# Kernel optimization log

Measured on AMD Instinct MI355X. Metric: run time of the kernel, lower is better.

The kernel has to match this reference:

```python
import jax, jax.numpy as jnp
import numpy as np

B, S, D, H = 4, 2048, 1024, 16
DK = D // H


def setup_inputs() -> dict:
    key = jax.random.key(0)
    ks = jax.random.split(key, 5)
    scale = 1.0 / np.sqrt(D)
    return {
        "x": jax.random.normal(ks[0], (B, S, D), dtype=jnp.float32),
        "mask": jnp.ones((1, 1, S, S), dtype=bool),
        "Wq": jax.random.normal(ks[1], (D, D), dtype=jnp.float32) * scale,
        "Wk": jax.random.normal(ks[2], (D, D), dtype=jnp.float32) * scale,
        "Wv": jax.random.normal(ks[3], (D, D), dtype=jnp.float32) * scale,
        "Wo": jax.random.normal(ks[4], (D, D), dtype=jnp.float32) * scale,
    }


def reference(x, mask, Wq, Wk, Wv, Wo):
    # nn.Linear(d_model, d_model, bias=False): y = x @ W.T
    q = jnp.einsum('bsd,ed->bse', x, Wq).reshape(B, S, H, DK).transpose(0, 2, 1, 3)
    k = jnp.einsum('bsd,ed->bse', x, Wk).reshape(B, S, H, DK).transpose(0, 2, 1, 3)
    v = jnp.einsum('bsd,ed->bse', x, Wv).reshape(B, S, H, DK).transpose(0, 2, 1, 3)
    # scaled dot-product attention: [B,H,S,S]
    scores = jnp.einsum('bhqd,bhkd->bhqk', q, k) / jnp.sqrt(jnp.float32(DK))
    scores = jnp.where(mask, scores, jnp.float32(-1e9))
    attn = jax.nn.softmax(scores, axis=-1)
    out = jnp.einsum('bhqk,bhkd->bhqd', attn, v)  # [B,H,S,DK]
    out = out.transpose(0, 2, 1, 3).reshape(B, S, D)
    return jnp.einsum('bsd,ed->bse', out, Wo)
```

## Files before the change

### kernel.cpp

```cpp
#include <hip/hip_runtime.h>

typedef __bf16 bf16x8 __attribute__((ext_vector_type(8)));
typedef float f32x4 __attribute__((ext_vector_type(4)));
typedef float f32x16 __attribute__((ext_vector_type(16)));
typedef unsigned short u16;
typedef unsigned short u16x8 __attribute__((ext_vector_type(8)));
typedef unsigned short u16x4 __attribute__((ext_vector_type(4)));
typedef unsigned int u32;
typedef unsigned int u32x4 __attribute__((ext_vector_type(4)));

#define MFMA16(a, b, c) __builtin_amdgcn_mfma_f32_16x16x32_bf16(a, b, c, 0, 0, 0)
#define MFMA32(a, b, c) __builtin_amdgcn_mfma_f32_32x32x16_bf16(a, b, c, 0, 0, 0)

#if defined(__has_builtin)
#if __has_builtin(__builtin_amdgcn_exp2f)
#define EXP2(x) __builtin_amdgcn_exp2f(x)
#endif
#endif
#ifndef EXP2
#define EXP2(x) exp2f(x)
#endif

constexpr int NB = 4, NH = 16, SEQ = 2048, DM = 1024, DKH = 64;
constexpr int MTOT = NB * SEQ;
constexpr size_t QKV_ELEMS = (size_t)MTOT * DM;
constexpr size_t W_ELEMS = (size_t)DM * DM;
constexpr float QSCALE = 0.125f * 1.44269504088896340736f;

__device__ __forceinline__ int swz(int row, int col, int rowlen) {
  return (row * rowlen + col) ^ ((row & 7) << 3);
}

__device__ __forceinline__ void gload16(const u16* g, u16* l) {
  __builtin_amdgcn_global_load_lds(
      (const __attribute__((address_space(1))) void*)g,
      (__attribute__((address_space(3))) void*)l, 16, 0, 0);
}

__device__ __forceinline__ u32 cvtpk(float lo, float hi) {
  u32 r;
  asm("v_cvt_pk_bf16_f32 %0, %1, %2" : "=v"(r) : "v"(lo), "v"(hi));
  return r;
}
__device__ __forceinline__ void plswap(u32& a, u32& b) {
  asm volatile("v_permlane32_swap_b32 %0, %1" : "+v"(a), "+v"(b));
}

__global__ __launch_bounds__(256) void convert_bf16(
    const float* __restrict__ X, const float* __restrict__ Wq,
    const float* __restrict__ Wk, const float* __restrict__ Wv,
    const float* __restrict__ Wo, u16* __restrict__ Xb,
    u16* __restrict__ Wqb, u16* __restrict__ Wkb, u16* __restrict__ Wvb,
    u16* __restrict__ Wob) {
  const int bid = blockIdx.x;
  const float* src;
  u16* dst;
  size_t base;
  if (bid < 4096) {
    src = X; dst = Xb; base = (size_t)bid * 2048;
  } else {
    const int t = (bid - 4096) >> 9, r = (bid - 4096) & 511;
    src = (t == 0) ? Wq : (t == 1) ? Wk : (t == 2) ? Wv : Wo;
    dst = (t == 0) ? Wqb : (t == 1) ? Wkb : (t == 2) ? Wvb : Wob;
    base = (size_t)r * 2048;
  }
  const size_t e = base + (size_t)threadIdx.x * 8;
  const float4 a = *reinterpret_cast<const float4*>(src + e);
  const float4 b = *reinterpret_cast<const float4*>(src + e + 4);
  bf16x8 v;
  v[0] = (__bf16)a.x; v[1] = (__bf16)a.y; v[2] = (__bf16)a.z; v[3] = (__bf16)a.w;
  v[4] = (__bf16)b.x; v[5] = (__bf16)b.y; v[6] = (__bf16)b.z; v[7] = (__bf16)b.w;
  *reinterpret_cast<bf16x8*>(dst + e) = v;
}

__global__ __launch_bounds__(256) void gemm_qkv(
    const u16* __restrict__ A, const u16* __restrict__ Wqb,
    const u16* __restrict__ Wkb, const u16* __restrict__ Wvb,
    u16* __restrict__ Qb, u16* __restrict__ Kb, u16* __restrict__ Vtb) {
  constexpr int BM = 128, BK = 64, NT = DM / BK;
  __shared__ __align__(16) u16 As[2][BM * BK];
  __shared__ __align__(16) u16 Bs[2][BM * BK];

  const int mode = blockIdx.y >> 3;
  const u16* B = (mode == 0) ? Wqb : (mode == 1) ? Wkb : Wvb;
  u16* Yz = (mode == 0) ? Qb : (mode == 1) ? Kb : Vtb;

  const int tid = threadIdx.x;
  const int lane = tid & 63, w = tid >> 6;
  const int ln = lane & 15, lg = lane >> 4;
  const int wr = (w >> 1) * 64, wc = (w & 1) * 64;
  const int m0 = blockIdx.x * BM, n0 = (blockIdx.y & 7) * BM;

  const int srow = tid >> 3;
  const int sgg = (tid & 7) ^ (srow & 7);
  const size_t aoff = (size_t)(m0 + srow) * DM + sgg * 8;
  const size_t boff = (size_t)(n0 + srow) * DM + sgg * 8;
  const int lbase = w * 512;

  f32x4 acc[4][4];
#pragma unroll
  for (int i = 0; i < 4; ++i)
#pragma unroll
    for (int j = 0; j < 4; ++j) acc[i][j] = (f32x4){0.f, 0.f, 0.f, 0.f};

  auto stage = [&](int bsel, int k0) {
#pragma unroll
    for (int c = 0; c < 4; ++c) {
      gload16(A + aoff + (size_t)c * 32 * DM + k0, &As[bsel][c * 2048 + lbase]);
      gload16(B + boff + (size_t)c * 32 * DM + k0, &Bs[bsel][c * 2048 + lbase]);
    }
  };

  stage(0, 0);
  __syncthreads();

  int buf = 0;
  for (int t = 0; t < NT; ++t) {
    if (t + 1 < NT) stage(buf ^ 1, (t + 1) * BK);
    if (mode == 2) {
#pragma unroll
      for (int kc = 0; kc < 2; ++kc) {
        bf16x8 af[4], bfr[4];
#pragma unroll
        for (int i = 0; i < 4; ++i)
          af[i] = *reinterpret_cast<const bf16x8*>(
              &As[buf][swz(wr + i * 16 + ln, kc * 32 + lg * 8, BK)]);
#pragma unroll
        for (int j = 0; j < 4; ++j)
          bfr[j] = *reinterpret_cast<const bf16x8*>(
              &Bs[buf][swz(wc + j * 16 + ln, kc * 32 + lg * 8, BK)]);
#pragma unroll
        for (int i = 0; i < 4; ++i)
#pragma unroll
          for (int j = 0; j < 4; ++j) acc[i][j] = MFMA16(af[i], bfr[j], acc[i][j]);
      }
    } else {
#pragma unroll
      for (int kc = 0; kc < 2; ++kc) {
        bf16x8 af[4], bfr[4];
#pragma unroll
        for (int i = 0; i < 4; ++i)
          af[i] = *reinterpret_cast<const bf16x8*>(
              &As[buf][swz(wr + i * 16 + ln, kc * 32 + lg * 8, BK)]);
#pragma unroll
        for (int j = 0; j < 4; ++j)
          bfr[j] = *reinterpret_cast<const bf16x8*>(
              &Bs[buf][swz(wc + j * 16 + ln, kc * 32 + lg * 8, BK)]);
#pragma unroll
        for (int i = 0; i < 4; ++i)
#pragma unroll
          for (int j = 0; j < 4; ++j) acc[i][j] = MFMA16(bfr[j], af[i], acc[i][j]);
      }
    }
    __syncthreads();
    buf ^= 1;
  }

  if (mode == 2) {
#pragma unroll
    for (int i = 0; i < 4; ++i) {
      const int mB = m0 + wr + i * 16 + lg * 4;
      const int bb = mB >> 11, s0 = mB & (SEQ - 1);
#pragma unroll
      for (int j = 0; j < 4; ++j) {
        const int n = n0 + wc + j * 16 + ln;
        const int h = n >> 6, dk = n & 63;
        u16x4 ov;
#pragma unroll
        for (int r = 0; r < 4; ++r)
          ov[r] = __builtin_bit_cast(u16, (__bf16)acc[i][j][r]);
        *reinterpret_cast<u16x4*>(
            &Yz[(((size_t)(bb * NH + h)) * DKH + dk) * SEQ + s0]) = ov;
      }
    }
  } else {
    const float sc = (mode == 0) ? QSCALE : 1.0f;
#pragma unroll
    for (int i = 0; i < 4; ++i) {
      const int m = m0 + wr + i * 16 + ln;
      const int bb = m >> 11, s = m & (SEQ - 1);
#pragma unroll
      for (int j = 0; j < 4; ++j) {
        const int nb = n0 + wc + j * 16 + lg * 4;
        const int h = nb >> 6, dk0 = nb & 63;
        u16x4 ov;
#pragma unroll
        for (int r = 0; r < 4; ++r)
          ov[r] = __builtin_bit_cast(u16, (__bf16)(acc[i][j][r] * sc));
        *reinterpret_cast<u16x4*>(
            &Yz[(((size_t)(bb * NH + h)) * SEQ + s) * DKH + dk0]) = ov;
      }
    }
  }
}

__global__ __launch_bounds__(256) void gemm_out(
    const u16* __restrict__ A, const u16* __restrict__ B,
    float* __restrict__ Out) {
  constexpr int BM = 128, BK = 64, NT = DM / BK;
  __shared__ __align__(16) u16 As[2][BM * BK];
  __shared__ __align__(16) u16 Bs[2][BM * BK];

  const int tid = threadIdx.x;
  const int lane = tid & 63, w = tid >> 6;
  const int ln = lane & 15, lg = lane >> 4;
  const int wr = (w >> 1) * 64, wc = (w & 1) * 64;
  const int m0 = blockIdx.x * BM, n0 = blockIdx.y * BM;

  const int srow = tid >> 3;
  const int sgg = (tid & 7) ^ (srow & 7);
  const size_t aoff = (size_t)(m0 + srow) * DM + sgg * 8;
  const size_t boff = (size_t)(n0 + srow) * DM + sgg * 8;
  const int lbase = w * 512;

  f32x4 acc[4][4];
#pragma unroll
  for (int i = 0; i < 4; ++i)
#pragma unroll
    for (int j = 0; j < 4; ++j) acc[i][j] = (f32x4){0.f, 0.f, 0.f, 0.f};

  auto stage = [&](int bsel, int k0) {
#pragma unroll
    for (int c = 0; c < 4; ++c) {
      gload16(A + aoff + (size_t)c * 32 * DM + k0, &As[bsel][c * 2048 + lbase]);
      gload16(B + boff + (size_t)c * 32 * DM + k0, &Bs[bsel][c * 2048 + lbase]);
    }
  };

  stage(0, 0);
  __syncthreads();

  int buf = 0;
  for (int t = 0; t < NT; ++t) {
    if (t + 1 < NT) stage(buf ^ 1, (t + 1) * BK);
#pragma unroll
    for (int kc = 0; kc < 2; ++kc) {
      bf16x8 af[4], bfr[4];
#pragma unroll
      for (int i = 0; i < 4; ++i)
        af[i] = *reinterpret_cast<const bf16x8*>(
            &As[buf][swz(wr + i * 16 + ln, kc * 32 + lg * 8, BK)]);
#pragma unroll
      for (int j = 0; j < 4; ++j)
        bfr[j] = *reinterpret_cast<const bf16x8*>(
            &Bs[buf][swz(wc + j * 16 + ln, kc * 32 + lg * 8, BK)]);
#pragma unroll
      for (int i = 0; i < 4; ++i)
#pragma unroll
        for (int j = 0; j < 4; ++j) acc[i][j] = MFMA16(bfr[j], af[i], acc[i][j]);
    }
    __syncthreads();
    buf ^= 1;
  }

#pragma unroll
  for (int i = 0; i < 4; ++i) {
    const int m = m0 + wr + i * 16 + ln;
#pragma unroll
    for (int j = 0; j < 4; ++j) {
      const int nb = n0 + wc + j * 16 + lg * 4;
      float4 v = {acc[i][j][0], acc[i][j][1], acc[i][j][2], acc[i][j][3]};
      *reinterpret_cast<float4*>(&Out[(size_t)m * DM + nb]) = v;
    }
  }
}

__global__ __launch_bounds__(256, 4) void attn_fwd(
    const u16* __restrict__ Qg, const u16* __restrict__ Kg,
    const u16* __restrict__ Vg, u16* __restrict__ Og) {
  constexpr int KVB = 64, NT = SEQ / KVB;
  const int bid = blockIdx.x;
  const int xcd = bid & 7, grp = bid >> 3;
  const int bh = xcd * 8 + (grp >> 4), qt = grp & 15;
  const int b = bh >> 4, h = bh & 15;
  const int tid = threadIdx.x, lane = tid & 63, wv = tid >> 6;
  const int l31 = lane & 31, hi = lane >> 5;
  const size_t hoff = (size_t)bh * SEQ * DKH;
  const u16* __restrict__ Qh = Qg + hoff;
  const u16* __restrict__ Kh = Kg + hoff;
  const u16* __restrict__ Vth = Vg + hoff;

  __shared__ __align__(16) u16 Ks[2][8 * 512];
  __shared__ __align__(16) u16 Vs[2][8 * 512];

  const int qbase = qt * 128 + wv * 32;

  bf16x8 qf[4];
#pragma unroll
  for (int c = 0; c < 4; ++c)
    qf[c] = *reinterpret_cast<const bf16x8*>(
        Qh + (size_t)(qbase + l31) * DKH + c * 16 + hi * 8);

  bf16x8 ones;
#pragma unroll
  for (int e = 0; e < 8; ++e) ones[e] = (__bf16)1.0f;

  float mrow = -1e30f;
  f32x16 ot[2], lacc;
#pragma unroll
  for (int i = 0; i < 16; ++i) { ot[0][i] = 0.f; ot[1][i] = 0.f; lacc[i] = 0.f; }

  const u16* sK0 = Kh + (size_t)l31 * DKH + wv * 16 + hi * 8;
  const u16* sK1 = sK0 + 32 * DKH;
  const u16* sV0 = Vth + (size_t)l31 * SEQ + wv * 16 + hi * 8;
  const u16* sV1 = sV0 + (size_t)32 * SEQ;

  auto stage = [&](int bsel, int kv0) {
    gload16(sK0 + (size_t)kv0 * DKH, &Ks[bsel][wv * 512]);
    gload16(sK1 + (size_t)kv0 * DKH, &Ks[bsel][(wv + 4) * 512]);
    gload16(sV0 + kv0, &Vs[bsel][wv * 512]);
    gload16(sV1 + kv0, &Vs[bsel][(wv + 4) * 512]);
  };

  stage(0, 0);
  __syncthreads();

  int buf = 0;
  for (int t = 0; t < NT; ++t) {
    if (t + 1 < NT) stage(buf ^ 1, (t + 1) * KVB);
    const u16* ksb = Ks[buf];
    const u16* vsb = Vs[buf];

    f32x16 sf[2];
#pragma unroll
    for (int i = 0; i < 16; ++i) { sf[0][i] = 0.f; sf[1][i] = 0.f; }

    __builtin_amdgcn_s_setprio(1);
#pragma unroll
    for (int ks = 0; ks < 2; ++ks)
#pragma unroll
      for (int c = 0; c < 4; ++c) {
        bf16x8 ka = *reinterpret_cast<const bf16x8*>(
            &ksb[(ks * 4 + c) * 512 + lane * 8]);
        sf[ks] = MFMA32(ka, qf[c], sf[ks]);
      }
    __builtin_amdgcn_s_setprio(0);

    float t8[8];
#pragma unroll
    for (int i = 0; i < 8; ++i)
      t8[i] = fmaxf(fmaxf(sf[0][i], sf[0][i + 8]),
                    fmaxf(sf[1][i], sf[1][i + 8]));
    float ta = fmaxf(fmaxf(t8[0], t8[1]), t8[2]);
    float tb = fmaxf(fmaxf(t8[3], t8[4]), t8[5]);
    float tc = fmaxf(fmaxf(t8[6], t8[7]), ta);
    float pm = fmaxf(tb, tc);
    pm = fmaxf(pm, __shfl_xor(pm, 32));

    if (__any(pm > mrow + 8.f)) {
      const float mn = fmaxf(mrow, pm);
      const float corr = EXP2(mrow - mn);
      mrow = mn;
      lacc *= corr;
      ot[0] *= corr;
      ot[1] *= corr;
    }
    sf[0] = sf[0] - mrow;
    sf[1] = sf[1] - mrow;
#pragma unroll
    for (int ks = 0; ks < 2; ++ks)
#pragma unroll
      for (int i = 0; i < 16; ++i) sf[ks][i] = EXP2(sf[ks][i]);

#pragma unroll
    for (int ks = 0; ks < 2; ++ks) {
#pragma unroll
      for (int hk = 0; hk < 2; ++hk) {
        u32 wA0 = cvtpk(sf[ks][8 * hk + 0], sf[ks][8 * hk + 1]);
        u32 wA1 = cvtpk(sf[ks][8 * hk + 2], sf[ks][8 * hk + 3]);
        u32 wB0 = cvtpk(sf[ks][8 * hk + 4], sf[ks][8 * hk + 5]);
        u32 wB1 = cvtpk(sf[ks][8 * hk + 6], sf[ks][8 * hk + 7]);
        plswap(wA0, wB0);
        plswap(wA1, wB1);
        u32x4 pw;
        pw[0] = wA0; pw[1] = wA1; pw[2] = wB0; pw[3] = wB1;
        const bf16x8 pb = __builtin_bit_cast(bf16x8, pw);
        const int kc = ks * 2 + hk;
        __builtin_amdgcn_s_setprio(1);
        bf16x8 va0 = *reinterpret_cast<const bf16x8*>(
            &vsb[(0 * 4 + kc) * 512 + lane * 8]);
        bf16x8 va1 = *reinterpret_cast<const bf16x8*>(
            &vsb[(1 * 4 + kc) * 512 + lane * 8]);
        ot[0] = MFMA32(va0, pb, ot[0]);
        ot[1] = MFMA32(va1, pb, ot[1]);
        lacc = MFMA32(ones, pb, lacc);
        __builtin_amdgcn_s_setprio(0);
      }
    }

    __syncthreads();
    buf ^= 1;
  }

  const float inv = 1.f / lacc[0];
  const int q = qbase + l31;
#pragma unroll
  for (int ds = 0; ds < 2; ++ds)
#pragma unroll
    for (int blk = 0; blk < 4; ++blk) {
      u16x4 ov;
#pragma unroll
      for (int r = 0; r < 4; ++r)
        ov[r] = __builtin_bit_cast(u16, (__bf16)(ot[ds][blk * 4 + r] * inv));
      const int d0 = ds * 32 + blk * 8 + hi * 4;
      *reinterpret_cast<u16x4*>(
          &Og[((size_t)(b * SEQ + q)) * DM + h * DKH + d0]) = ov;
    }
}

extern "C" void kernel_launch(void* const* d_in, const int* in_sizes, int n_in,
                              void* d_out, int out_size, void* d_ws, size_t ws_size,
                              hipStream_t stream) {
  const float* x  = (const float*)d_in[0];
  const float* Wq = (const float*)d_in[2];
  const float* Wk = (const float*)d_in[3];
  const float* Wv = (const float*)d_in[4];
  const float* Wo = (const float*)d_in[5];
  float* out = (float*)d_out;

  u16* Xb  = (u16*)d_ws;
  u16* Wqb = Xb + QKV_ELEMS;
  u16* Wkb = Wqb + W_ELEMS;
  u16* Wvb = Wkb + W_ELEMS;
  u16* Wob = Wvb + W_ELEMS;
  u16* Kb  = Wob + W_ELEMS;
  u16* Vtb = Kb + QKV_ELEMS;
  u16* Qb  = (u16*)d_out;
  u16* Obuf = Xb;

  convert_bf16<<<6144, 256, 0, stream>>>(x, Wq, Wk, Wv, Wo,
                                         Xb, Wqb, Wkb, Wvb, Wob);
  gemm_qkv<<<dim3(MTOT / 128, 24), 256, 0, stream>>>(Xb, Wqb, Wkb, Wvb,
                                                     Qb, Kb, Vtb);
  attn_fwd<<<dim3(NB * NH * 16), 256, 0, stream>>>(Qb, Kb, Vtb, Obuf);
  gemm_out<<<dim3(MTOT / 128, DM / 128), 256, 0, stream>>>(Obuf, Wob, out);
}
```

Baseline: 208.8 us.

## Use 512-thread attention blocks with 4-stage KV ring and one barrier per tile

Each attention block now has 8 waves and covers 256 query rows, so K/V tiles loaded into shared memory are shared by twice as many waves, which halves the global K/V traffic per query. The double buffer becomes a 4-slot ring with three tiles in flight, using explicit vmcnt waits and a single barrier per iteration in place of two __syncthreads. The cost is larger LDS per block (64KB), fewer blocks in the grid, and correctness that depends on the hand-counted vmcnt values matching the issued loads.

```diff
diff --git a/kernel.cpp b/kernel.cpp
--- a/kernel.cpp
+++ b/kernel.cpp
@@ -265,13 +265,13 @@
   }
 }
 
-__global__ __launch_bounds__(256, 4) void attn_fwd(
+__global__ __launch_bounds__(512, 4) void attn_fwd(
     const u16* __restrict__ Qg, const u16* __restrict__ Kg,
     const u16* __restrict__ Vg, u16* __restrict__ Og) {
   constexpr int KVB = 64, NT = SEQ / KVB;
   const int bid = blockIdx.x;
   const int xcd = bid & 7, grp = bid >> 3;
-  const int bh = xcd * 8 + (grp >> 4), qt = grp & 15;
+  const int bh = xcd * 8 + (grp >> 3), qt = grp & 7;
   const int b = bh >> 4, h = bh & 15;
   const int tid = threadIdx.x, lane = tid & 63, wv = tid >> 6;
   const int l31 = lane & 31, hi = lane >> 5;
@@ -280,10 +280,10 @@
   const u16* __restrict__ Kh = Kg + hoff;
   const u16* __restrict__ Vth = Vg + hoff;
 
-  __shared__ __align__(16) u16 Ks[2][8 * 512];
-  __shared__ __align__(16) u16 Vs[2][8 * 512];
-
-  const int qbase = qt * 128 + wv * 32;
+  __shared__ __align__(16) u16 Ks[4][8 * 512];
+  __shared__ __align__(16) u16 Vs[4][8 * 512];
+
+  const int qbase = qt * 256 + wv * 32;
 
   bf16x8 qf[4];
 #pragma unroll
@@ -300,26 +300,30 @@
 #pragma unroll
   for (int i = 0; i < 16; ++i) { ot[0][i] = 0.f; ot[1][i] = 0.f; lacc[i] = 0.f; }
 
-  const u16* sK0 = Kh + (size_t)l31 * DKH + wv * 16 + hi * 8;
-  const u16* sK1 = sK0 + 32 * DKH;
-  const u16* sV0 = Vth + (size_t)l31 * SEQ + wv * 16 + hi * 8;
-  const u16* sV1 = sV0 + (size_t)32 * SEQ;
+  const u16* sK = Kh + (size_t)((wv >> 2) * 32 + l31) * DKH + (wv & 3) * 16 + hi * 8;
+  const u16* sV = Vth + (size_t)((wv >> 2) * 32 + l31) * SEQ + (wv & 3) * 16 + hi * 8;
 
   auto stage = [&](int bsel, int kv0) {
-    gload16(sK0 + (size_t)kv0 * DKH, &Ks[bsel][wv * 512]);
-    gload16(sK1 + (size_t)kv0 * DKH, &Ks[bsel][(wv + 4) * 512]);
-    gload16(sV0 + kv0, &Vs[bsel][wv * 512]);
-    gload16(sV1 + kv0, &Vs[bsel][(wv + 4) * 512]);
+    gload16(sK + (size_t)kv0 * DKH, &Ks[bsel][wv * 512]);
+    gload16(sV + kv0, &Vs[bsel][wv * 512]);
   };
 
   stage(0, 0);
-  __syncthreads();
-
-  int buf = 0;
+  asm volatile("" ::: "memory");
+  stage(1, KVB);
+  asm volatile("" ::: "memory");
+  stage(2, 2 * KVB);
+
+  int cur = 0;
   for (int t = 0; t < NT; ++t) {
-    if (t + 1 < NT) stage(buf ^ 1, (t + 1) * KVB);
-    const u16* ksb = Ks[buf];
-    const u16* vsb = Vs[buf];
+    if (t < NT - 2) asm volatile("s_waitcnt vmcnt(4)" ::: "memory");
+    else if (t == NT - 2) asm volatile("s_waitcnt vmcnt(2)" ::: "memory");
+    else asm volatile("s_waitcnt vmcnt(0)" ::: "memory");
+    __builtin_amdgcn_s_barrier();
+    if (t + 3 < NT) stage((cur + 3) & 3, (t + 3) * KVB);
+
+    const u16* ksb = Ks[cur];
+    const u16* vsb = Vs[cur];
 
     f32x16 sf[2];
 #pragma unroll
@@ -388,8 +392,7 @@
       }
     }
 
-    __syncthreads();
-    buf ^= 1;
+    cur = (cur + 1) & 3;
   }
 
   const float inv = 1.f / lacc[0];
@@ -432,6 +435,6 @@
                                          Xb, Wqb, Wkb, Wvb, Wob);
   gemm_qkv<<<dim3(MTOT / 128, 24), 256, 0, stream>>>(Xb, Wqb, Wkb, Wvb,
                                                      Qb, Kb, Vtb);
-  attn_fwd<<<dim3(NB * NH * 16), 256, 0, stream>>>(Qb, Kb, Vtb, Obuf);
+  attn_fwd<<<dim3(NB * NH * 8), 512, 0, stream>>>(Qb, Kb, Vtb, Obuf);
   gemm_out<<<dim3(MTOT / 128, DM / 128), 256, 0, stream>>>(Obuf, Wob, out);
 }
```

New measurement: 202.4 us. 1.03x faster.
